# Kernel optimization log

Hardware: AMD Instinct MI355X
Metric: run time of the kernel (lower is better)

Reference implementation:

```python
import jax, jax.numpy as jnp
import numpy as np

B, C, H, W = 4, 256, 64, 64
PD = 32  # projection_dim = in_channels // projection_ratio


def setup_inputs() -> dict:
    key = jax.random.key(0)
    ks = jax.random.split(key, 7)
    x = jax.random.normal(ks[0], (B, C, H, W), dtype=jnp.float32)
    Wq = jax.random.normal(ks[1], (PD, C), dtype=jnp.float32) * (1.0 / np.sqrt(C))
    bq = jax.random.normal(ks[2], (PD,), dtype=jnp.float32) * 0.01
    Wk = jax.random.normal(ks[3], (PD, C), dtype=jnp.float32) * (1.0 / np.sqrt(C))
    bk = jax.random.normal(ks[4], (PD,), dtype=jnp.float32) * 0.01
    Wv = jax.random.normal(ks[5], (C, C), dtype=jnp.float32) * (1.0 / np.sqrt(C))
    bv = jax.random.normal(ks[6], (C,), dtype=jnp.float32) * 0.01
    gamma = jnp.float32(1.0)
    return {"x": x, "Wq": Wq, "bq": bq, "Wk": Wk, "bk": bk, "Wv": Wv, "bv": bv, "gamma": gamma}


def reference(x, Wq, bq, Wk, bk, Wv, bv, gamma):
    b, c, h, w = x.shape
    xf = x.reshape(b, c, h * w)                      # [B, C, N]
    q = jnp.einsum('dc,bcn->bnd', Wq, xf) + bq       # [B, N, PD]
    k = jnp.einsum('dc,bcn->bdn', Wk, xf) + bk[:, None]   # [B, PD, N]
    v = jnp.einsum('ec,bcn->ben', Wv, xf) + bv[:, None]   # [B, C, N]
    scores = jnp.einsum('bnd,bdm->bnm', q, k)        # [B, N, N] (no scaling, per original)
    attn = jax.nn.softmax(scores, axis=-1)           # softmax over keys
    out = jnp.einsum('bcn,bmn->bcm', v, attn)        # v @ attn^T -> [B, C, N]
    out = out.reshape(b, c, h, w)
    return gamma * out + x
```

## Files before the change

kernel.cpp:

```cpp
#include <hip/hip_runtime.h>
#include <stdint.h>

typedef _Float16 half_t;
typedef __attribute__((ext_vector_type(8))) _Float16 f16x8;
typedef __attribute__((ext_vector_type(4))) _Float16 f16x4;
typedef __attribute__((ext_vector_type(2))) __fp16 fp16x2;
typedef __attribute__((ext_vector_type(4))) float f32x4;
typedef __attribute__((ext_vector_type(16))) float f32x16;
typedef __attribute__((ext_vector_type(4))) uint32_t u32x4;
typedef __attribute__((ext_vector_type(2))) int i32x2;

#define DEVI __device__ __forceinline__

static constexpr int Bn = 4, Cc = 256, Nn = 4096, PD = 32;
static constexpr float L2E = 1.44269504089f;

__device__ half_t g_Q[(size_t)Bn * Nn * PD];
__device__ half_t g_K[(size_t)Bn * Nn * PD];
__device__ half_t g_V[(size_t)Bn * Cc * Nn];

DEVI f16x8 cvt8(float4 a, float4 b) {
    f16x8 r;
    r[0] = (_Float16)a.x; r[1] = (_Float16)a.y; r[2] = (_Float16)a.z; r[3] = (_Float16)a.w;
    r[4] = (_Float16)b.x; r[5] = (_Float16)b.y; r[6] = (_Float16)b.z; r[7] = (_Float16)b.w;
    return r;
}

DEVI uint32_t pkrtz(float a, float b) {
    fp16x2 h = __builtin_amdgcn_cvt_pkrtz(a, b);
    return __builtin_bit_cast(uint32_t, h);
}

DEVI float asf(int u) { return __builtin_bit_cast(float, u); }
DEVI int   asi(float f) { return __builtin_bit_cast(int, f); }

DEVI i32x2 pl32swap(int a, int b) {
    return __builtin_amdgcn_permlane32_swap(a, b, false, false);
}

DEVI void gll16(const void* g, void* l) {
    auto gp = (const __attribute__((address_space(1))) uint32_t*)(uintptr_t)g;
    auto lp = (__attribute__((address_space(3))) uint32_t*)(uintptr_t)l;
    __builtin_amdgcn_global_load_lds(gp, lp, 16, 0, 0);
}

__global__ __launch_bounds__(256, 1) void proj_kernel(
    const float* __restrict__ x,
    const float* __restrict__ Wq, const float* __restrict__ bq,
    const float* __restrict__ Wk, const float* __restrict__ bk,
    const float* __restrict__ Wv, const float* __restrict__ bv)
{
    __shared__ __align__(16) half_t xt[64 * 40];

    const int b    = blockIdx.x >> 6;
    const int n0   = (blockIdx.x & 63) * 64;
    const int t    = threadIdx.x;
    const int w    = t >> 6;
    const int lane = t & 63;
    const int l15  = lane & 15, g = lane >> 4;

    f32x4 qk_acc[4] = {};
    f32x4 v_acc[4][4] = {};

    const float* wrow_qk = (w < 2) ? (Wq + (size_t)(16 * w + l15) * Cc)
                                   : (Wk + (size_t)(16 * (w - 2) + l15) * Cc);

    for (int cs = 0; cs < 8; ++cs) {
        const int c0 = cs * 32;
        {
            const int nl = t & 63;
            const int cg = t >> 6;
            const float* xp = x + ((size_t)(b * Cc + c0 + cg * 8)) * Nn + n0 + nl;
            float f[8];
#pragma unroll
            for (int q = 0; q < 8; ++q) f[q] = xp[(size_t)q * Nn];
            f16x4 h0, h1;
#pragma unroll
            for (int q = 0; q < 4; ++q) { h0[q] = (_Float16)f[q]; h1[q] = (_Float16)f[q + 4]; }
            *(f16x4*)&xt[nl * 40 + cg * 8]     = h0;
            *(f16x4*)&xt[nl * 40 + cg * 8 + 4] = h1;
        }
        __syncthreads();

        f16x8 xf[4];
#pragma unroll
        for (int nf = 0; nf < 4; ++nf)
            xf[nf] = *(const f16x8*)&xt[(nf * 16 + l15) * 40 + g * 8];

        {
            const float* wp = wrow_qk + c0 + g * 8;
            const f16x8 af = cvt8(*(const float4*)wp, *(const float4*)(wp + 4));
#pragma unroll
            for (int nt = 0; nt < 4; ++nt)
                qk_acc[nt] = __builtin_amdgcn_mfma_f32_16x16x32_f16(af, xf[nt], qk_acc[nt], 0, 0, 0);
        }
#pragma unroll
        for (int et = 0; et < 4; ++et) {
            const int e = (w * 4 + et) * 16 + l15;
            const float* wp = Wv + (size_t)e * Cc + c0 + g * 8;
            const f16x8 wf = cvt8(*(const float4*)wp, *(const float4*)(wp + 4));
#pragma unroll
            for (int nf = 0; nf < 4; ++nf)
                v_acc[et][nf] = __builtin_amdgcn_mfma_f32_16x16x32_f16(xf[nf], wf, v_acc[et][nf], 0, 0, 0);
        }
        __syncthreads();
    }

    {
        const float* bias = (w < 2) ? bq : bk;
        const int dbase = 16 * (w & 1) + 4 * g;
        float bb[4];
#pragma unroll
        for (int r = 0; r < 4; ++r) bb[r] = bias[dbase + r];
        half_t* dst = (w < 2) ? g_Q : g_K;
#pragma unroll
        for (int nt = 0; nt < 4; ++nt) {
            const int n = n0 + nt * 16 + l15;
            f16x4 h;
#pragma unroll
            for (int r = 0; r < 4; ++r) h[r] = (_Float16)(qk_acc[nt][r] + bb[r]);
            *(f16x4*)&dst[((size_t)b * Nn + n) * PD + dbase] = h;
        }
    }
#pragma unroll
    for (int et = 0; et < 4; ++et) {
        const int e = (w * 4 + et) * 16 + l15;
        const float bve = bv[e];
#pragma unroll
        for (int nf = 0; nf < 4; ++nf) {
            const int n = n0 + nf * 16 + 4 * g;
            f16x4 h;
#pragma unroll
            for (int r = 0; r < 4; ++r) h[r] = (_Float16)(v_acc[et][nf][r] + bve);
            *(f16x4*)&g_V[((size_t)b * Cc + e) * Nn + n] = h;
        }
    }
}

__global__ __launch_bounds__(512, 2) void attn_kernel(
    const float* __restrict__ x, const float* __restrict__ gamma_p, float* __restrict__ out)
{
    __shared__ __align__(16) half_t V_lds[2][256 * 128];
    __shared__ float mx[2][4][32];
    __shared__ float lx[2][4][32];

    const int blk = blockIdx.x;
    const int grp = blk & 7;
    const int b   = grp >> 1;
    const int mt  = ((blk >> 3) << 1) | (grp & 1);

    const int t    = threadIdx.x;
    const int w    = t >> 6;
    const int lane = t & 63;
    const int l31  = lane & 31;
    const int hi   = lane >> 5;
    const int kk   = w & 3;
    const int mh   = w >> 2;
    const int mrow0 = mt * 64 + mh * 32;

    const half_t* Kb  = g_K + (size_t)b * Nn * PD;
    const half_t* Vbg = g_V + (size_t)b * Cc * Nn;

    const half_t* qp = g_Q + ((size_t)b * Nn + mrow0 + l31) * PD + hi * 8;
    const f16x8 q0 = *(const f16x8*)qp;
    const f16x8 q1 = *(const f16x8*)(qp + 16);

    const int vr = w * 4 + (lane >> 4);
    const half_t* vb = Vbg + (size_t)vr * Nn + (((lane & 15) ^ (vr & 7)) * 8);

    const int e7   = l31 & 7;
    const int off0 = (((kk * 4) + hi) ^ e7) * 8;
    const int off1 = (((kk * 4) + 2 + hi) ^ e7) * 8;

    f32x16 acc[8] = {};
    float run_m = -1e30f, run_l = 0.f;
    const f32x16 zero16 = {};

    f16x8 pa0, pa1;
    f16x8 kq0, kq1;
    float alpha = 1.f;
    bool  needscale = false;

    auto softmax_pack = [&](const f32x16& sn, f16x8& o0, f16x8& o1) {
        float m01 = fmaxf(sn[0], sn[1]),   m23 = fmaxf(sn[2], sn[3]);
        float m45 = fmaxf(sn[4], sn[5]),   m67 = fmaxf(sn[6], sn[7]);
        float m89 = fmaxf(sn[8], sn[9]),   mab = fmaxf(sn[10], sn[11]);
        float mcd = fmaxf(sn[12], sn[13]), mef = fmaxf(sn[14], sn[15]);
        float tm = fmaxf(fmaxf(fmaxf(m01, m23), fmaxf(m45, m67)),
                         fmaxf(fmaxf(m89, mab), fmaxf(mcd, mef)));
        {
            const i32x2 rr = pl32swap(asi(tm), asi(tm));
            tm = fmaxf(asf(rr[0]), asf(rr[1]));
        }
        needscale = __any(tm > run_m + 8.f);
        if (needscale) {
            const float nm = fmaxf(run_m, tm);
            alpha = __builtin_amdgcn_exp2f((run_m - nm) * L2E);
            run_m = nm;
        } else {
            alpha = 1.f;
        }
        const float nms = run_m * L2E;
        float p[16];
#pragma unroll
        for (int r = 0; r < 16; ++r)
            p[r] = __builtin_amdgcn_exp2f(sn[r] * L2E - nms);
        float rs = (((p[0] + p[1]) + (p[2] + p[3])) + ((p[4] + p[5]) + (p[6] + p[7])))
                 + (((p[8] + p[9]) + (p[10] + p[11])) + ((p[12] + p[13]) + (p[14] + p[15])));
        {
            const i32x2 rr = pl32swap(asi(rs), asi(rs));
            rs = asf(rr[0]) + asf(rr[1]);
        }
        run_l = run_l * alpha + rs;
        {
            const i32x2 r0 = pl32swap((int)pkrtz(p[0], p[1]), (int)pkrtz(p[4], p[5]));
            const i32x2 r1 = pl32swap((int)pkrtz(p[2], p[3]), (int)pkrtz(p[6], p[7]));
            u32x4 d0 = {(uint32_t)r0[0], (uint32_t)r1[0], (uint32_t)r0[1], (uint32_t)r1[1]};
            o0 = __builtin_bit_cast(f16x8, d0);
            const i32x2 r2 = pl32swap((int)pkrtz(p[8], p[9]),   (int)pkrtz(p[12], p[13]));
            const i32x2 r3 = pl32swap((int)pkrtz(p[10], p[11]), (int)pkrtz(p[14], p[15]));
            u32x4 d1 = {(uint32_t)r2[0], (uint32_t)r3[0], (uint32_t)r2[1], (uint32_t)r3[1]};
            o1 = __builtin_bit_cast(f16x8, d1);
        }
    };

    {
        const half_t* kp0 = Kb + (size_t)(kk * 32 + l31) * PD + hi * 8;
        const f16x8 ka = *(const f16x8*)kp0;
        const f16x8 kb = *(const f16x8*)(kp0 + 16);
        f32x16 s0 = __builtin_amdgcn_mfma_f32_32x32x16_f16(ka, q0, zero16, 0, 0, 0);
        s0 = __builtin_amdgcn_mfma_f32_32x32x16_f16(kb, q1, s0, 0, 0, 0);
        softmax_pack(s0, pa0, pa1);
        needscale = false;
    }
#pragma unroll
    for (int rr = 0; rr < 8; ++rr)
        gll16(vb + (size_t)rr * 32 * Nn, &V_lds[0][rr * 4096 + w * 512]);
    __builtin_amdgcn_sched_barrier(0);
    const half_t* kp = Kb + (size_t)(128 + kk * 32 + l31) * PD + hi * 8;
    kq0 = *(const f16x8*)kp;
    kq1 = *(const f16x8*)(kp + 16);
    __builtin_amdgcn_sched_barrier(0);

    constexpr int NT = Nn / 128;
    for (int i = 0; i < NT - 1; ++i) {
        const int buf = i & 1;

        asm volatile("s_waitcnt vmcnt(2)" ::: "memory");
        __builtin_amdgcn_s_barrier();
        __builtin_amdgcn_sched_barrier(0);

        if (needscale) {
#pragma unroll
            for (int r = 0; r < 16; ++r) {
                const float ar = __shfl(alpha, (r & 3) + 8 * (r >> 2) + 4 * hi);
#pragma unroll
                for (int et = 0; et < 8; ++et) acc[et][r] *= ar;
            }
        }

        f32x16 sn = __builtin_amdgcn_mfma_f32_32x32x16_f16(kq0, q0, zero16, 0, 0, 0);
        sn = __builtin_amdgcn_mfma_f32_32x32x16_f16(kq1, q1, sn, 0, 0, 0);

#pragma unroll
        for (int rr = 0; rr < 8; ++rr)
            gll16(vb + 128 + (size_t)rr * 32 * Nn, &V_lds[buf ^ 1][rr * 4096 + w * 512]);
        vb += 128;

        __builtin_amdgcn_s_setprio(1);
#pragma unroll
        for (int et = 0; et < 4; ++et) {
            const int rowb = (et * 32 + l31) * 128;
            const f16x8 vf0 = *(const f16x8*)&V_lds[buf][rowb + off0];
            const f16x8 vf1 = *(const f16x8*)&V_lds[buf][rowb + off1];
            acc[et] = __builtin_amdgcn_mfma_f32_32x32x16_f16(pa0, vf0, acc[et], 0, 0, 0);
            acc[et] = __builtin_amdgcn_mfma_f32_32x32x16_f16(pa1, vf1, acc[et], 0, 0, 0);
        }
        __builtin_amdgcn_s_setprio(0);

        f16x8 pn0, pn1;
        softmax_pack(sn, pn0, pn1);

        __builtin_amdgcn_s_setprio(1);
#pragma unroll
        for (int et = 4; et < 8; ++et) {
            const int rowb = (et * 32 + l31) * 128;
            const f16x8 vf0 = *(const f16x8*)&V_lds[buf][rowb + off0];
            const f16x8 vf1 = *(const f16x8*)&V_lds[buf][rowb + off1];
            acc[et] = __builtin_amdgcn_mfma_f32_32x32x16_f16(pa0, vf0, acc[et], 0, 0, 0);
            acc[et] = __builtin_amdgcn_mfma_f32_32x32x16_f16(pa1, vf1, acc[et], 0, 0, 0);
        }
        __builtin_amdgcn_s_setprio(0);

        pa0 = pn0;
        pa1 = pn1;

        kp += 128 * PD;
        if (i + 2 >= NT) kp = Kb + (size_t)(kk * 32 + l31) * PD + hi * 8;
        kq0 = *(const f16x8*)kp;
        kq1 = *(const f16x8*)(kp + 16);
        __builtin_amdgcn_sched_barrier(0);
    }

    {
        const int buf = (NT - 1) & 1;
        asm volatile("s_waitcnt vmcnt(2)" ::: "memory");
        __builtin_amdgcn_s_barrier();
        __builtin_amdgcn_sched_barrier(0);
        if (needscale) {
#pragma unroll
            for (int r = 0; r < 16; ++r) {
                const float ar = __shfl(alpha, (r & 3) + 8 * (r >> 2) + 4 * hi);
#pragma unroll
                for (int et = 0; et < 8; ++et) acc[et][r] *= ar;
            }
        }
        __builtin_amdgcn_s_setprio(1);
#pragma unroll
        for (int et = 0; et < 8; ++et) {
            const int rowb = (et * 32 + l31) * 128;
            const f16x8 vf0 = *(const f16x8*)&V_lds[buf][rowb + off0];
            const f16x8 vf1 = *(const f16x8*)&V_lds[buf][rowb + off1];
            acc[et] = __builtin_amdgcn_mfma_f32_32x32x16_f16(pa0, vf0, acc[et], 0, 0, 0);
            acc[et] = __builtin_amdgcn_mfma_f32_32x32x16_f16(pa1, vf1, acc[et], 0, 0, 0);
        }
        __builtin_amdgcn_s_setprio(0);
    }

    if (lane < 32) { mx[mh][kk][l31] = run_m; lx[mh][kk][l31] = run_l; }
    __syncthreads();

    float sc16[16], li16[16];
    {
        const float m0 = mx[mh][0][l31], m1 = mx[mh][1][l31];
        const float m2 = mx[mh][2][l31], m3 = mx[mh][3][l31];
        const float M  = fmaxf(fmaxf(m0, m1), fmaxf(m2, m3));
        const float L  = lx[mh][0][l31] * __builtin_amdgcn_exp2f((m0 - M) * L2E)
                       + lx[mh][1][l31] * __builtin_amdgcn_exp2f((m1 - M) * L2E)
                       + lx[mh][2][l31] * __builtin_amdgcn_exp2f((m2 - M) * L2E)
                       + lx[mh][3][l31] * __builtin_amdgcn_exp2f((m3 - M) * L2E);
        const float ssf = __builtin_amdgcn_exp2f((run_m - M) * L2E);
        const float inv = 1.0f / L;
#pragma unroll
        for (int r = 0; r < 16; ++r) {
            const int src = (r & 3) + 8 * (r >> 2) + 4 * hi;
            sc16[r] = __shfl(ssf, src);
            li16[r] = __shfl(inv, src);
        }
    }
    __syncthreads();

    const float gm = gamma_p[0];
    float4* mrg = (float4*)&V_lds[0][0];
#pragma unroll
    for (int h = 0; h < 2; ++h) {
#pragma unroll
        for (int j = 0; j < 4; ++j) {
            const int et = h * 4 + j;
#pragma unroll
            for (int q = 0; q < 4; ++q) {
                float4 v;
                v.x = acc[et][4 * q + 0] * sc16[4 * q + 0];
                v.y = acc[et][4 * q + 1] * sc16[4 * q + 1];
                v.z = acc[et][4 * q + 2] * sc16[4 * q + 2];
                v.w = acc[et][4 * q + 3] * sc16[4 * q + 3];
                mrg[((w * 4 + j) * 4 + q) * 64 + lane] = v;
            }
        }
        __syncthreads();
        {
            const int et = h * 4 + kk;
            const int e  = et * 32 + l31;
#pragma unroll
            for (int q = 0; q < 4; ++q) {
                float4 s0 = mrg[(((mh * 4 + 0) * 4 + kk) * 4 + q) * 64 + lane];
                float4 s1 = mrg[(((mh * 4 + 1) * 4 + kk) * 4 + q) * 64 + lane];
                float4 s2 = mrg[(((mh * 4 + 2) * 4 + kk) * 4 + q) * 64 + lane];
                float4 s3 = mrg[(((mh * 4 + 3) * 4 + kk) * 4 + q) * 64 + lane];
                const size_t idx = ((size_t)b * Cc + e) * Nn + mrow0 + 8 * q + 4 * hi;
                const float4 xin = *(const float4*)&x[idx];
                float4 o;
                o.x = gm * (s0.x + s1.x + s2.x + s3.x) * li16[4 * q + 0] + xin.x;
                o.y = gm * (s0.y + s1.y + s2.y + s3.y) * li16[4 * q + 1] + xin.y;
                o.z = gm * (s0.z + s1.z + s2.z + s3.z) * li16[4 * q + 2] + xin.z;
                o.w = gm * (s0.w + s1.w + s2.w + s3.w) * li16[4 * q + 3] + xin.w;
                *(float4*)&out[idx] = o;
            }
        }
        __syncthreads();
    }
}

extern "C" void kernel_launch(void* const* d_in, const int* in_sizes, int n_in,
                              void* d_out, int out_size, void* d_ws, size_t ws_size,
                              hipStream_t stream) {
    (void)in_sizes; (void)n_in; (void)out_size; (void)d_ws; (void)ws_size;
    const float* x  = (const float*)d_in[0];
    const float* Wq = (const float*)d_in[1];
    const float* bq = (const float*)d_in[2];
    const float* Wk = (const float*)d_in[3];
    const float* bk = (const float*)d_in[4];
    const float* Wv = (const float*)d_in[5];
    const float* bv = (const float*)d_in[6];
    const float* gm = (const float*)d_in[7];
    float* out = (float*)d_out;

    proj_kernel<<<256, 256, 0, stream>>>(x, Wq, bq, Wk, bk, Wv, bv);
    attn_kernel<<<256, 512, 0, stream>>>(x, gm, out);
}
```

Measured before the change: 91.26 us.

## Stagger softmax and PV MFMA phases between two wave groups per block

Splits waves by mh into two schedules. One group does the softmax at the start of each tile and then a full block of PV MFMAs. The other group issues the PV MFMAs first and does the softmax afterward. The aim is for one group's exp/VALU work to overlap the other group's matrix-core work, in a ping-pong style, instead of each wave interleaving both. It also folds the epilogue into the main loop through a 'more' flag. The risk is extra register pressure from the pending score tile and divergent code paths.

```diff
diff --git a/kernel.cpp b/kernel.cpp
--- a/kernel.cpp
+++ b/kernel.cpp
@@ -176,6 +176,7 @@
     float run_m = -1e30f, run_l = 0.f;
     const f32x16 zero16 = {};
 
+    f32x16 s;
     f16x8 pa0, pa1;
     f16x8 kq0, kq1;
     float alpha = 1.f;
@@ -224,14 +225,21 @@
         }
     };
 
+    auto rescale_acc = [&]() {
+#pragma unroll
+        for (int r = 0; r < 16; ++r) {
+            const float ar = __shfl(alpha, (r & 3) + 8 * (r >> 2) + 4 * hi);
+#pragma unroll
+            for (int et = 0; et < 8; ++et) acc[et][r] *= ar;
+        }
+    };
+
     {
         const half_t* kp0 = Kb + (size_t)(kk * 32 + l31) * PD + hi * 8;
         const f16x8 ka = *(const f16x8*)kp0;
         const f16x8 kb = *(const f16x8*)(kp0 + 16);
-        f32x16 s0 = __builtin_amdgcn_mfma_f32_32x32x16_f16(ka, q0, zero16, 0, 0, 0);
-        s0 = __builtin_amdgcn_mfma_f32_32x32x16_f16(kb, q1, s0, 0, 0, 0);
-        softmax_pack(s0, pa0, pa1);
-        needscale = false;
+        s = __builtin_amdgcn_mfma_f32_32x32x16_f16(ka, q0, zero16, 0, 0, 0);
+        s = __builtin_amdgcn_mfma_f32_32x32x16_f16(kb, q1, s, 0, 0, 0);
     }
 #pragma unroll
     for (int rr = 0; rr < 8; ++rr)
@@ -241,90 +249,86 @@
     kq0 = *(const f16x8*)kp;
     kq1 = *(const f16x8*)(kp + 16);
     __builtin_amdgcn_sched_barrier(0);
+    if (mh == 1) {
+        softmax_pack(s, pa0, pa1);
+        needscale = false;
+    }
 
     constexpr int NT = Nn / 128;
-    for (int i = 0; i < NT - 1; ++i) {
+    for (int i = 0; i < NT; ++i) {
         const int buf = i & 1;
+        const bool more = (i + 1 < NT);
 
         asm volatile("s_waitcnt vmcnt(2)" ::: "memory");
         __builtin_amdgcn_s_barrier();
         __builtin_amdgcn_sched_barrier(0);
 
-        if (needscale) {
-#pragma unroll
-            for (int r = 0; r < 16; ++r) {
-                const float ar = __shfl(alpha, (r & 3) + 8 * (r >> 2) + 4 * hi);
-#pragma unroll
-                for (int et = 0; et < 8; ++et) acc[et][r] *= ar;
-            }
-        }
-
-        f32x16 sn = __builtin_amdgcn_mfma_f32_32x32x16_f16(kq0, q0, zero16, 0, 0, 0);
-        sn = __builtin_amdgcn_mfma_f32_32x32x16_f16(kq1, q1, sn, 0, 0, 0);
-
-#pragma unroll
-        for (int rr = 0; rr < 8; ++rr)
-            gll16(vb + 128 + (size_t)rr * 32 * Nn, &V_lds[buf ^ 1][rr * 4096 + w * 512]);
-        vb += 128;
-
-        __builtin_amdgcn_s_setprio(1);
-#pragma unroll
-        for (int et = 0; et < 4; ++et) {
-            const int rowb = (et * 32 + l31) * 128;
-            const f16x8 vf0 = *(const f16x8*)&V_lds[buf][rowb + off0];
-            const f16x8 vf1 = *(const f16x8*)&V_lds[buf][rowb + off1];
-            acc[et] = __builtin_amdgcn_mfma_f32_32x32x16_f16(pa0, vf0, acc[et], 0, 0, 0);
-            acc[et] = __builtin_amdgcn_mfma_f32_32x32x16_f16(pa1, vf1, acc[et], 0, 0, 0);
-        }
-        __builtin_amdgcn_s_setprio(0);
-
-        f16x8 pn0, pn1;
-        softmax_pack(sn, pn0, pn1);
-
-        __builtin_amdgcn_s_setprio(1);
-#pragma unroll
-        for (int et = 4; et < 8; ++et) {
-            const int rowb = (et * 32 + l31) * 128;
-            const f16x8 vf0 = *(const f16x8*)&V_lds[buf][rowb + off0];
-            const f16x8 vf1 = *(const f16x8*)&V_lds[buf][rowb + off1];
-            acc[et] = __builtin_amdgcn_mfma_f32_32x32x16_f16(pa0, vf0, acc[et], 0, 0, 0);
-            acc[et] = __builtin_amdgcn_mfma_f32_32x32x16_f16(pa1, vf1, acc[et], 0, 0, 0);
-        }
-        __builtin_amdgcn_s_setprio(0);
-
-        pa0 = pn0;
-        pa1 = pn1;
-
-        kp += 128 * PD;
-        if (i + 2 >= NT) kp = Kb + (size_t)(kk * 32 + l31) * PD + hi * 8;
-        kq0 = *(const f16x8*)kp;
-        kq1 = *(const f16x8*)(kp + 16);
-        __builtin_amdgcn_sched_barrier(0);
-    }
-
-    {
-        const int buf = (NT - 1) & 1;
-        asm volatile("s_waitcnt vmcnt(2)" ::: "memory");
-        __builtin_amdgcn_s_barrier();
-        __builtin_amdgcn_sched_barrier(0);
-        if (needscale) {
-#pragma unroll
-            for (int r = 0; r < 16; ++r) {
-                const float ar = __shfl(alpha, (r & 3) + 8 * (r >> 2) + 4 * hi);
-#pragma unroll
-                for (int et = 0; et < 8; ++et) acc[et][r] *= ar;
-            }
-        }
-        __builtin_amdgcn_s_setprio(1);
-#pragma unroll
-        for (int et = 0; et < 8; ++et) {
-            const int rowb = (et * 32 + l31) * 128;
-            const f16x8 vf0 = *(const f16x8*)&V_lds[buf][rowb + off0];
-            const f16x8 vf1 = *(const f16x8*)&V_lds[buf][rowb + off1];
-            acc[et] = __builtin_amdgcn_mfma_f32_32x32x16_f16(pa0, vf0, acc[et], 0, 0, 0);
-            acc[et] = __builtin_amdgcn_mfma_f32_32x32x16_f16(pa1, vf1, acc[et], 0, 0, 0);
-        }
-        __builtin_amdgcn_s_setprio(0);
+        if (mh == 0) {
+            softmax_pack(s, pa0, pa1);
+            if (needscale) rescale_acc();
+
+            if (more) {
+#pragma unroll
+                for (int rr = 0; rr < 8; ++rr)
+                    gll16(vb + 128 + (size_t)rr * 32 * Nn, &V_lds[buf ^ 1][rr * 4096 + w * 512]);
+                vb += 128;
+            }
+            __builtin_amdgcn_sched_barrier(0);
+
+            __builtin_amdgcn_s_setprio(1);
+#pragma unroll
+            for (int et = 0; et < 8; ++et) {
+                const int rowb = (et * 32 + l31) * 128;
+                const f16x8 vf0 = *(const f16x8*)&V_lds[buf][rowb + off0];
+                const f16x8 vf1 = *(const f16x8*)&V_lds[buf][rowb + off1];
+                acc[et] = __builtin_amdgcn_mfma_f32_32x32x16_f16(pa0, vf0, acc[et], 0, 0, 0);
+                acc[et] = __builtin_amdgcn_mfma_f32_32x32x16_f16(pa1, vf1, acc[et], 0, 0, 0);
+            }
+            __builtin_amdgcn_s_setprio(0);
+
+            if (more) {
+                s = __builtin_amdgcn_mfma_f32_32x32x16_f16(kq0, q0, zero16, 0, 0, 0);
+                s = __builtin_amdgcn_mfma_f32_32x32x16_f16(kq1, q1, s, 0, 0, 0);
+                kp += 128 * PD;
+                if (i + 2 >= NT) kp = Kb + (size_t)(kk * 32 + l31) * PD + hi * 8;
+                kq0 = *(const f16x8*)kp;
+                kq1 = *(const f16x8*)(kp + 16);
+                __builtin_amdgcn_sched_barrier(0);
+            }
+        } else {
+            if (needscale) rescale_acc();
+
+            f32x16 sn;
+            if (more) {
+                sn = __builtin_amdgcn_mfma_f32_32x32x16_f16(kq0, q0, zero16, 0, 0, 0);
+                sn = __builtin_amdgcn_mfma_f32_32x32x16_f16(kq1, q1, sn, 0, 0, 0);
+#pragma unroll
+                for (int rr = 0; rr < 8; ++rr)
+                    gll16(vb + 128 + (size_t)rr * 32 * Nn, &V_lds[buf ^ 1][rr * 4096 + w * 512]);
+                vb += 128;
+            }
+            __builtin_amdgcn_sched_barrier(0);
+
+            __builtin_amdgcn_s_setprio(1);
+#pragma unroll
+            for (int et = 0; et < 8; ++et) {
+                const int rowb = (et * 32 + l31) * 128;
+                const f16x8 vf0 = *(const f16x8*)&V_lds[buf][rowb + off0];
+                const f16x8 vf1 = *(const f16x8*)&V_lds[buf][rowb + off1];
+                acc[et] = __builtin_amdgcn_mfma_f32_32x32x16_f16(pa0, vf0, acc[et], 0, 0, 0);
+                acc[et] = __builtin_amdgcn_mfma_f32_32x32x16_f16(pa1, vf1, acc[et], 0, 0, 0);
+            }
+            __builtin_amdgcn_s_setprio(0);
+
+            if (more) {
+                softmax_pack(sn, pa0, pa1);
+                kp += 128 * PD;
+                if (i + 2 >= NT) kp = Kb + (size_t)(kk * 32 + l31) * PD + hi * 8;
+                kq0 = *(const f16x8*)kp;
+                kq1 = *(const f16x8*)(kp + 16);
+                __builtin_amdgcn_sched_barrier(0);
+            }
+        }
     }
 
     if (lane < 32) { mx[mh][kk][l31] = run_m; lx[mh][kk][l31] = run_l; }
```

Result: no change. 91.52 us (+0.3%).
